# Performance work log

Hardware: AMD Instinct MI355X
Metric: run time of the kernel (lower is better)

Reference implementation:

```python
import jax, jax.numpy as jnp
import numpy as np
from jax.scipy.special import digamma

K = 3
N_CLASSES = 10
HIGH_CST = 1e7


def setup_inputs() -> dict:
    key = jax.random.key(0)
    k1, k2 = jax.random.split(key)
    X = jax.random.normal(k1, (8192, 128), dtype=jnp.float32)
    y = jax.random.randint(k2, (8192,), 0, N_CLASSES, dtype=jnp.int64)
    return {"X": X, "y": y}


def _pairwise_euclidean(X):
    sq = jnp.sum(X * X, axis=1)
    d2 = sq[:, None] - 2.0 * (X @ X.T) + sq[None, :]
    return jnp.sqrt(jnp.maximum(d2, 0.0))


def reference(X, y):
    N = X.shape[0]
    N_digamma = digamma(jnp.asarray(N, dtype=jnp.float32))

    # per-class counts N_x and weighted digamma average
    y32 = y.astype(jnp.int32)
    N_x = jnp.bincount(y32, length=N_CLASSES).astype(jnp.float32)
    avg_N_x = jnp.sum((N_x / N) * digamma(N_x))

    dists = _pairwise_euclidean(X)  # [N, N]

    # mask out different-class pairs with a huge constant
    same_class = y[:, None] == y[None, :]
    dists_same = jnp.where(same_class, dists, HIGH_CST)

    # k-th same-class neighbor distance (self included at distance 0 -> take k+1 smallest, last)
    neg_top, _ = jax.lax.top_k(-dists_same, K + 1)
    anchor_dists = -neg_top[:, -1]  # [N]

    # count all points (any class) within that radius, excluding self
    m_i = jnp.sum(dists <= anchor_dists[:, None], axis=1) - 1
    avg_m_i = jnp.mean(digamma(m_i.astype(jnp.float32)))

    k_digamma = digamma(jnp.asarray(K, dtype=jnp.float32))
    mi = N_digamma - avg_N_x + k_digamma - avg_m_i
    return jnp.maximum(mi / jnp.log(jnp.asarray(2.0, dtype=jnp.float32)), 0.0)
```

## Files before the change

kernel.cpp:

```cpp
#include <hip/hip_runtime.h>
#include <hip/hip_bf16.h>
#include <math.h>

#define NCLS 10
#define NTOT 8192
#define NTIL 64
#define NJT 8
#define NJG (NTOT / (128 * NJT))
#define NPMAX 9472
#define MAXSLOT 32
#define G1 2560

using short8 = __attribute__((ext_vector_type(8))) short;
using f32x4  = __attribute__((ext_vector_type(4))) float;

__device__ __forceinline__ float digammaf_dev(float x) {
    float r = 0.0f;
    while (x < 6.0f) { r -= 1.0f / x; x += 1.0f; }
    float inv = 1.0f / x;
    float inv2 = inv * inv;
    float s = logf(x) - 0.5f * inv
            - inv2 * (0.083333333333f - inv2 * (0.0083333333333f - inv2 * 0.0039682539683f));
    return r + s;
}

__device__ __forceinline__ void cmpswap(float& a, float& b) {
    float lo = fminf(a, b), hi = fmaxf(a, b);
    a = lo; b = hi;
}

__device__ __forceinline__ void ins7(float v, float& b0, float& b1, float& b2, float& b3) {
    float x0 = fminf(b0, v); float c0 = fmaxf(b0, v);
    float x1 = fminf(b1, c0); float c1 = fmaxf(b1, c0);
    float x2 = fminf(b2, c1); float c2 = fmaxf(b2, c1);
    float x3 = fminf(b3, c2);
    b0 = x0; b1 = x1; b2 = x2; b3 = x3;
}

__device__ __forceinline__ void bmerge(int mk, float& v0, float& v1, float& v2, float& v3) {
    float u0 = __shfl_xor(v0, mk), u1 = __shfl_xor(v1, mk);
    float u2 = __shfl_xor(v2, mk), u3 = __shfl_xor(v3, mk);
    float m0 = fminf(v0, u3), m1 = fminf(v1, u2);
    float m2 = fminf(v2, u1), m3 = fminf(v3, u0);
    cmpswap(m0, m2); cmpswap(m1, m3);
    cmpswap(m0, m1); cmpswap(m2, m3);
    v0 = m0; v1 = m1; v2 = m2; v3 = m3;
}

__device__ __forceinline__ void gload_lds16(const void* g, void* s) {
    __builtin_amdgcn_global_load_lds((const __attribute__((address_space(1))) void*)g,
                                     (__attribute__((address_space(3))) void*)s, 16, 0, 0);
}

__global__ void prep_kernel(const float* __restrict__ X,
                            float* __restrict__ sq, unsigned short* __restrict__ XS) {
    int wave = threadIdx.x >> 6, lane = threadIdx.x & 63;
    int row = blockIdx.x * 4 + wave;
    float2 v = *(const float2*)(X + (size_t)row * 128 + lane * 2);
    __hip_bfloat16 h0 = __float2bfloat16(v.x);
    __hip_bfloat16 h1 = __float2bfloat16(v.y);
    float hf0 = __bfloat162float(h0), hf1 = __bfloat162float(h1);
    __hip_bfloat16 l0 = __float2bfloat16(v.x - hf0);
    __hip_bfloat16 l1 = __float2bfloat16(v.y - hf1);
    ushort2 hp, lp;
    hp.x = *(unsigned short*)&h0; hp.y = *(unsigned short*)&h1;
    lp.x = *(unsigned short*)&l0; lp.y = *(unsigned short*)&l1;
    *(ushort2*)(XS + (size_t)row * 256 + lane * 2) = hp;
    *(ushort2*)(XS + (size_t)row * 256 + 128 + lane * 2) = lp;
    float s = fmaf(v.x, v.x, v.y * v.y);
    #pragma unroll
    for (int off = 32; off > 0; off >>= 1) s += __shfl_down(s, off);
    if (lane == 0) sq[row] = s;
}

__global__ void count_kernel(const int* __restrict__ y, int* __restrict__ bcnt) {
    __shared__ int hist[NCLS];
    int t = threadIdx.x;
    if (t < NCLS) hist[t] = 0;
    __syncthreads();
    atomicAdd(&hist[y[blockIdx.x * 256 + t]], 1);
    __syncthreads();
    if (t < NCLS) bcnt[blockIdx.x * NCLS + t] = hist[t];
}

__global__ void plan_kernel(const int* __restrict__ bcnt, int* __restrict__ plan,
                            int* __restrict__ sOff, int* __restrict__ cls) {
    __shared__ int sT[NCLS], sBase[NCLS];
    const int c = threadIdx.x;
    if (c < NCLS) {
        int run = 0;
        #pragma unroll 8
        for (int b = 0; b < 32; ++b) {
            sOff[b * NCLS + c] = run;
            run += bcnt[b * NCLS + c];
        }
        cls[c] = run;
        sT[c] = (run + 127) >> 7;
    }
    __syncthreads();
    if (c == 0) {
        int rowBase = 0, cum = 0;
        for (int q = 0; q < NCLS; ++q) {
            int T = sT[q];
            int nsl = (T + 1) >> 1;
            sBase[q] = rowBase;
            plan[q] = rowBase;
            plan[10 + q] = T;
            plan[20 + q] = nsl;
            plan[30 + q] = cum;
            rowBase += T << 7;
            cum += T * nsl;
        }
        plan[40] = cum;
    }
    __syncthreads();
    if (c < NCLS) {
        int rb = sBase[c];
        #pragma unroll 8
        for (int b = 0; b < 32; ++b) sOff[b * NCLS + c] += rb;
    }
}

__global__ void init_yP(int* __restrict__ yP) {
    yP[blockIdx.x * 256 + threadIdx.x] = -1;
}

__global__ void scatter_kernel(const int* __restrict__ y, const float* __restrict__ sq,
                               const unsigned short* __restrict__ XS,
                               const int* __restrict__ sOff,
                               unsigned short* __restrict__ XSP, float* __restrict__ sqP,
                               int* __restrict__ yP, int* __restrict__ idxP) {
    __shared__ int yloc[256];
    __shared__ int dstloc[256];
    const int b = blockIdx.x, t = threadIdx.x;
    const int gid = b * 256 + t;
    const int yv = y[gid];
    yloc[t] = yv;
    __syncthreads();
    int rank = 0;
    for (int k = 0; k < 256; ++k) rank += (k < t && yloc[k] == yv) ? 1 : 0;
    const int dst = sOff[b * NCLS + yv] + rank;
    dstloc[t] = dst;
    sqP[dst] = sq[gid];
    yP[dst] = yv;
    idxP[dst] = gid;
    __syncthreads();
    const int w = t >> 6, l = t & 63;
    for (int r = w; r < 256; r += 4) {
        int d = dstloc[r];
        *(ushort4*)(XSP + (size_t)d * 256 + l * 4) =
            *(const ushort4*)(XS + (size_t)(b * 256 + r) * 256 + l * 4);
    }
}

__global__ __launch_bounds__(256, 2)
void pass1_kernel(const unsigned short* __restrict__ XSP, const int* __restrict__ yP,
                  const float* __restrict__ sqP, const int* __restrict__ plan,
                  float* __restrict__ top4pP) {
    const int bid = blockIdx.x;
    if (bid >= plan[40]) return;
    __shared__ __align__(16) char smem[65536];

    const int t = threadIdx.x;
    const int w = t >> 6, l = t & 63;
    const int wr = w >> 1, wc = w & 1;
    const int lg = l >> 4, lo16 = l & 15;

    int cc = 0;
    #pragma unroll
    for (int q = 1; q < NCLS; ++q) if (bid >= plan[30 + q]) cc = q;
    const int rowBase = plan[cc], T = plan[10 + cc], nsl = plan[20 + cc];
    const int local = bid - plan[30 + cc];
    const int itile = local / nsl, sIdx = local % nsl;
    const int ibase = rowBase + itile * 128;

    float sqi[16]; int yi[16];
    #pragma unroll
    for (int mi = 0; mi < 4; ++mi)
        #pragma unroll
        for (int r = 0; r < 4; ++r) {
            int row = ibase + wr * 64 + mi * 16 + lg * 4 + r;
            sqi[mi * 4 + r] = sqP[row];
            yi[mi * 4 + r] = yP[row];
        }

    const int swz = (lo16 & 7) << 4;
    unsigned aoff[2], boff[2];
    #pragma unroll
    for (int kk = 0; kk < 2; ++kk) {
        const int cA = (kk * 64 + lg * 16) ^ swz;
        aoff[kk] = (unsigned)((wr * 64 + lo16) * 128 + cA);
        boff[kk] = (unsigned)(32768 + (wc * 64 + lo16) * 128 + cA);
    }
    const int srow = w * 32 + (l >> 3);
    const int scol = ((l & 7) ^ (l >> 3)) << 3;
    const unsigned short* gsrc = XSP + (size_t)srow * 256 + scol;

    auto STAGE = [&](int jbase_rows, int ks, int par) {
        if (ks < 2 || ks >= 4) {
            const int kA = (ks < 4) ? (ks & 1) * 64 : (ks - 2) * 64;
            char* Ab = smem + par * 16384 + w * 4096;
            const unsigned short* gA = gsrc + (size_t)ibase * 256 + kA;
            #pragma unroll
            for (int q = 0; q < 4; ++q)
                gload_lds16(gA + (size_t)q * 8 * 256, Ab + q * 1024);
        }
        const int kB = (ks < 4) ? ks * 64 : (ks - 4) * 64;
        char* Bb = smem + 32768 + par * 16384 + w * 4096;
        const unsigned short* gB = gsrc + (size_t)jbase_rows * 256 + kB;
        #pragma unroll
        for (int q = 0; q < 4; ++q)
            gload_lds16(gB + (size_t)q * 8 * 256, Bb + q * 1024);
    };

    float tp0[16], tp1[16], tp2[16], tp3[16];
    #pragma unroll
    for (int c = 0; c < 16; ++c) {
        tp0[c] = 1e30f; tp1[c] = 1e30f; tp2[c] = 1e30f; tp3[c] = 1e30f;
    }

    STAGE(rowBase + sIdx * 128, 0, 0);
    __syncthreads();

    #pragma unroll 1
    for (int jt = sIdx; jt < T; jt += nsl) {
        const int jbase = rowBase + jt * 128;
        float sqj[4]; int yj[4];
        #pragma unroll
        for (int ni = 0; ni < 4; ++ni) {
            int col = jbase + wc * 64 + ni * 16 + lo16;
            sqj[ni] = sqP[col];
            yj[ni] = yP[col];
        }
        f32x4 acc[4][4];
        f32x4 zz = {0.0f, 0.0f, 0.0f, 0.0f};
        #pragma unroll
        for (int mi = 0; mi < 4; ++mi)
            #pragma unroll
            for (int ni = 0; ni < 4; ++ni) acc[mi][ni] = zz;

        #pragma unroll
        for (int ks = 0; ks < 6; ++ks) {
            const int par = ks & 1;
            if (ks < 5) STAGE(jbase, ks + 1, par ^ 1);
            else if (jt + nsl < T) STAGE(rowBase + (jt + nsl) * 128, 0, par ^ 1);

            #pragma unroll
            for (int kk = 0; kk < 2; ++kk) {
                short8 aF[4], bF[4];
                #pragma unroll
                for (int mi = 0; mi < 4; ++mi)
                    aF[mi] = *(const short8*)(smem + aoff[kk] + par * 16384 + mi * 2048);
                #pragma unroll
                for (int ni = 0; ni < 4; ++ni)
                    bF[ni] = *(const short8*)(smem + boff[kk] + par * 16384 + ni * 2048);
                #pragma unroll
                for (int mi = 0; mi < 4; ++mi)
                    #pragma unroll
                    for (int ni = 0; ni < 4; ++ni)
                        acc[mi][ni] = __builtin_amdgcn_mfma_f32_16x16x32_bf16(
                            aF[mi], bF[ni], acc[mi][ni], 0, 0, 0);
            }

            if (ks == 5) {
                #pragma unroll
                for (int mi = 0; mi < 4; ++mi)
                    #pragma unroll
                    for (int r = 0; r < 4; ++r) {
                        const int idx = mi * 4 + r;
                        #pragma unroll
                        for (int ni = 0; ni < 4; ++ni) {
                            float d2 = fmaf(-2.0f, acc[mi][ni][r], sqi[idx] + sqj[ni]);
                            d2 = fmaxf(d2, 0.0f);
                            float v = (yi[idx] == yj[ni]) ? d2 : 1e30f;
                            ins7(v, tp0[idx], tp1[idx], tp2[idx], tp3[idx]);
                        }
                    }
            }
            __syncthreads();
        }
    }

    float* scrR = (float*)smem;
    #pragma unroll
    for (int idx = 0; idx < 16; ++idx) {
        float v0 = tp0[idx], v1 = tp1[idx], v2 = tp2[idx], v3 = tp3[idx];
        bmerge(1, v0, v1, v2, v3); bmerge(2, v0, v1, v2, v3);
        bmerge(4, v0, v1, v2, v3); bmerge(8, v0, v1, v2, v3);
        if (lo16 == 0) {
            int rl = wr * 64 + (idx >> 2) * 16 + lg * 4 + (idx & 3);
            float4 st; st.x = v0; st.y = v1; st.z = v2; st.w = v3;
            *(float4*)(scrR + rl * 8 + wc * 4) = st;
        }
    }
    __syncthreads();
    if (t < 128) {
        float4 qa = *(float4*)(scrR + t * 8);
        float4 qb = *(float4*)(scrR + t * 8 + 4);
        float b0 = qa.x, b1 = qa.y, b2 = qa.z, b3 = qa.w;
        ins7(qb.x, b0, b1, b2, b3); ins7(qb.y, b0, b1, b2, b3);
        ins7(qb.z, b0, b1, b2, b3); ins7(qb.w, b0, b1, b2, b3);
        size_t base = ((size_t)(ibase + t) * MAXSLOT + sIdx) * 4;
        top4pP[base + 0] = b0; top4pP[base + 1] = b1;
        top4pP[base + 2] = b2; top4pP[base + 3] = b3;
    }
}

__global__ void anchorP_kernel(const float* __restrict__ top4pP, const int* __restrict__ yP,
                               const int* __restrict__ idxP, const int* __restrict__ plan,
                               float* __restrict__ anchor) {
    int r = blockIdx.x * 256 + threadIdx.x;
    int yv = yP[r];
    if (yv < 0) return;
    int nsl = plan[20 + yv];
    float b0 = 1e30f, b1 = 1e30f, b2 = 1e30f, b3 = 1e30f;
    const float4* q4 = (const float4*)(top4pP + (size_t)r * MAXSLOT * 4);
    for (int s = 0; s < nsl; ++s) {
        float4 q = q4[s];
        ins7(q.x, b0, b1, b2, b3); ins7(q.y, b0, b1, b2, b3);
        ins7(q.z, b0, b1, b2, b3); ins7(q.w, b0, b1, b2, b3);
    }
    anchor[idxP[r]] = b3;
}

__global__ __launch_bounds__(256, 2)
void pass2_kernel(const unsigned short* __restrict__ XS, const float* __restrict__ sq,
                  const float* __restrict__ anchor, int* __restrict__ cntp) {
    __shared__ __align__(16) char smem[65536];

    const int t = threadIdx.x;
    const int w = t >> 6, l = t & 63;
    const int wr = w >> 1, wc = w & 1;
    const int lg = l >> 4, lo16 = l & 15;

    const int bid = blockIdx.x;
    const int wg = (bid & 7) * ((NTIL * NJG) >> 3) + (bid >> 3);
    const int it = wg % NTIL, jg = wg / NTIL;
    const int ibase = it * 128;
    const int jg0 = jg * (128 * NJT);

    float sqi[16]; float anc[16];
    #pragma unroll
    for (int mi = 0; mi < 4; ++mi)
        #pragma unroll
        for (int r = 0; r < 4; ++r) {
            int row = ibase + wr * 64 + mi * 16 + lg * 4 + r;
            sqi[mi * 4 + r] = sq[row];
            anc[mi * 4 + r] = anchor[row];
        }

    const int swz = (lo16 & 7) << 4;
    unsigned aoff[2], boff[2];
    #pragma unroll
    for (int kk = 0; kk < 2; ++kk) {
        const int cA = (kk * 64 + lg * 16) ^ swz;
        aoff[kk] = (unsigned)((wr * 64 + lo16) * 128 + cA);
        boff[kk] = (unsigned)(32768 + (wc * 64 + lo16) * 128 + cA);
    }
    const int srow = w * 32 + (l >> 3);
    const int scol = ((l & 7) ^ (l >> 3)) << 3;
    const unsigned short* gsrc = XS + (size_t)srow * 256 + scol;

    auto STAGE = [&](int jbase_rows, int ks, int par) {
        if (ks < 2 || ks >= 4) {
            const int kA = (ks < 4) ? (ks & 1) * 64 : (ks - 2) * 64;
            char* Ab = smem + par * 16384 + w * 4096;
            const unsigned short* gA = gsrc + (size_t)ibase * 256 + kA;
            #pragma unroll
            for (int q = 0; q < 4; ++q)
                gload_lds16(gA + (size_t)q * 8 * 256, Ab + q * 1024);
        }
        const int kB = (ks < 4) ? ks * 64 : (ks - 4) * 64;
        char* Bb = smem + 32768 + par * 16384 + w * 4096;
        const unsigned short* gB = gsrc + (size_t)jbase_rows * 256 + kB;
        #pragma unroll
        for (int q = 0; q < 4; ++q)
            gload_lds16(gB + (size_t)q * 8 * 256, Bb + q * 1024);
    };

    int cnt16[16];
    #pragma unroll
    for (int c = 0; c < 16; ++c) cnt16[c] = 0;

    STAGE(jg0, 0, 0);
    __syncthreads();

    #pragma unroll 1
    for (int jt = 0; jt < NJT; ++jt) {
        const int jbase = jg0 + jt * 128;
        float sqj[4];
        #pragma unroll
        for (int ni = 0; ni < 4; ++ni)
            sqj[ni] = sq[jbase + wc * 64 + ni * 16 + lo16];

        f32x4 acc[4][4];
        f32x4 zz = {0.0f, 0.0f, 0.0f, 0.0f};
        #pragma unroll
        for (int mi = 0; mi < 4; ++mi)
            #pragma unroll
            for (int ni = 0; ni < 4; ++ni) acc[mi][ni] = zz;

        #pragma unroll
        for (int ks = 0; ks < 6; ++ks) {
            const int par = ks & 1;
            if (ks < 5) STAGE(jbase, ks + 1, par ^ 1);
            else if (jt < NJT - 1) STAGE(jbase + 128, 0, par ^ 1);

            #pragma unroll
            for (int kk = 0; kk < 2; ++kk) {
                short8 aF[4], bF[4];
                #pragma unroll
                for (int mi = 0; mi < 4; ++mi)
                    aF[mi] = *(const short8*)(smem + aoff[kk] + par * 16384 + mi * 2048);
                #pragma unroll
                for (int ni = 0; ni < 4; ++ni)
                    bF[ni] = *(const short8*)(smem + boff[kk] + par * 16384 + ni * 2048);
                #pragma unroll
                for (int mi = 0; mi < 4; ++mi)
                    #pragma unroll
                    for (int ni = 0; ni < 4; ++ni)
                        acc[mi][ni] = __builtin_amdgcn_mfma_f32_16x16x32_bf16(
                            aF[mi], bF[ni], acc[mi][ni], 0, 0, 0);
            }

            if (ks == 5) {
                #pragma unroll
                for (int mi = 0; mi < 4; ++mi)
                    #pragma unroll
                    for (int r = 0; r < 4; ++r) {
                        const int idx = mi * 4 + r;
                        int c = 0;
                        #pragma unroll
                        for (int ni = 0; ni < 4; ++ni) {
                            float d2 = fmaf(-2.0f, acc[mi][ni][r], sqi[idx] + sqj[ni]);
                            d2 = fmaxf(d2, 0.0f);
                            c += (d2 <= anc[idx]) ? 1 : 0;
                        }
                        cnt16[idx] += c;
                    }
            }
            __syncthreads();
        }
    }

    int* scri = (int*)smem;
    #pragma unroll
    for (int idx = 0; idx < 16; ++idx) {
        int c = cnt16[idx];
        c += __shfl_xor(c, 1); c += __shfl_xor(c, 2);
        c += __shfl_xor(c, 4); c += __shfl_xor(c, 8);
        if (lo16 == 0) {
            int rl = wr * 64 + (idx >> 2) * 16 + lg * 4 + (idx & 3);
            scri[rl * 2 + wc] = c;
        }
    }
    __syncthreads();
    if (t < 128) cntp[(size_t)(ibase + t) * NJG + jg] = scri[t * 2] + scri[t * 2 + 1];
}

__global__ void reduce_kernel(const int* __restrict__ cntp, float* __restrict__ partials) {
    __shared__ float red[256];
    int t = threadIdx.x;
    int row = blockIdx.x * 256 + t;
    int s = 0;
    for (int c = 0; c < NJG; ++c) s += cntp[(size_t)row * NJG + c];
    red[t] = digammaf_dev((float)(s - 1));
    __syncthreads();
    for (int h = 128; h > 0; h >>= 1) {
        if (t < h) red[t] += red[t + h];
        __syncthreads();
    }
    if (t == 0) partials[blockIdx.x] = red[0];
}

__global__ void finalize_kernel(const float* __restrict__ partials, const int* __restrict__ cls,
                                float* __restrict__ out) {
    if (threadIdx.x == 0) {
        float acc = 0.0f;
        for (int c = 0; c < NTOT / 256; ++c) acc += partials[c];
        float Nf = (float)NTOT;
        float avg_m = acc / Nf;
        float avgNx = 0.0f;
        for (int c = 0; c < NCLS; ++c) {
            float nx = (float)cls[c];
            if (nx > 0.0f) avgNx += (nx / Nf) * digammaf_dev(nx);
        }
        float mi = digammaf_dev(Nf) - avgNx + digammaf_dev(3.0f) - avg_m;
        out[0] = fmaxf(mi / logf(2.0f), 0.0f);
    }
}

extern "C" void kernel_launch(void* const* d_in, const int* in_sizes, int n_in,
                              void* d_out, int out_size, void* d_ws, size_t ws_size,
                              hipStream_t stream) {
    const float* X = (const float*)d_in[0];
    const int* y = (const int*)d_in[1];
    float* out = (float*)d_out;

    float* sq       = (float*)d_ws;
    float* anchors  = sq + NTOT;
    float* partials = anchors + NTOT;
    int*   cls      = (int*)(partials + 32);
    int*   bcnt     = cls + 16;
    int*   sOff     = bcnt + 320;
    int*   plan     = sOff + 320;
    int*   yP       = plan + 48;
    int*   idxP     = yP + NPMAX;
    float* sqP      = (float*)(idxP + NPMAX);
    unsigned short* XS  = (unsigned short*)(sqP + NPMAX);
    unsigned short* XSP = XS + (size_t)NTOT * 256;
    float* top4pP   = (float*)(XSP + (size_t)NPMAX * 256);
    int*   cntp     = (int*)(top4pP + (size_t)NPMAX * MAXSLOT * 4);

    prep_kernel<<<NTOT / 4, 256, 0, stream>>>(X, sq, XS);
    count_kernel<<<NTOT / 256, 256, 0, stream>>>(y, bcnt);
    plan_kernel<<<1, 64, 0, stream>>>(bcnt, plan, sOff, cls);
    init_yP<<<NPMAX / 256, 256, 0, stream>>>(yP);
    scatter_kernel<<<NTOT / 256, 256, 0, stream>>>(y, sq, XS, sOff, XSP, sqP, yP, idxP);
    pass1_kernel<<<G1, 256, 0, stream>>>(XSP, yP, sqP, plan, top4pP);
    anchorP_kernel<<<NPMAX / 256, 256, 0, stream>>>(top4pP, yP, idxP, plan, anchors);
    pass2_kernel<<<NTIL * NJG, 256, 0, stream>>>(XS, sq, anchors, cntp);
    reduce_kernel<<<NTOT / 256, 256, 0, stream>>>(cntp, partials);
    finalize_kernel<<<1, 64, 0, stream>>>(partials, cls, out);
}
```

Baseline: 133.9 us.

## Split pass1 into one block per 64x128 tile pair, fold yP init into plan

Pass1 now launches one block per (64-row i half-tile, 128-col j tile) pair within each class, so it no longer loops over j tiles. The grid grows to 2*T*T blocks per class, the A tile shrinks and LDS drops to 48KB. The goal is more parallelism and occupancy on the GPU and less per-block serial work. The cost is more blocks, repeated B loads and more partial top-4 writes (T slots per row instead of about T/2) that anchorP must merge. The yP initialisation is also folded into plan_kernel, which removes one launch.

```diff
diff --git a/kernel.cpp b/kernel.cpp
--- a/kernel.cpp
+++ b/kernel.cpp
@@ -9,7 +9,7 @@
 #define NJG (NTOT / (128 * NJT))
 #define NPMAX 9472
 #define MAXSLOT 32
-#define G1 2560
+#define G1 3072
 
 using short8 = __attribute__((ext_vector_type(8))) short;
 using f32x4  = __attribute__((ext_vector_type(4))) float;
@@ -84,9 +84,11 @@
 }
 
 __global__ void plan_kernel(const int* __restrict__ bcnt, int* __restrict__ plan,
-                            int* __restrict__ sOff, int* __restrict__ cls) {
+                            int* __restrict__ sOff, int* __restrict__ cls,
+                            int* __restrict__ yP) {
     __shared__ int sT[NCLS], sBase[NCLS];
     const int c = threadIdx.x;
+    for (int i = c; i < NPMAX; i += 256) yP[i] = -1;
     if (c < NCLS) {
         int run = 0;
         #pragma unroll 8
@@ -102,14 +104,13 @@
         int rowBase = 0, cum = 0;
         for (int q = 0; q < NCLS; ++q) {
             int T = sT[q];
-            int nsl = (T + 1) >> 1;
             sBase[q] = rowBase;
             plan[q] = rowBase;
             plan[10 + q] = T;
-            plan[20 + q] = nsl;
+            plan[20 + q] = T;
             plan[30 + q] = cum;
             rowBase += T << 7;
-            cum += T * nsl;
+            cum += 2 * T * T;
         }
         plan[40] = cum;
     }
@@ -119,10 +120,6 @@
         #pragma unroll 8
         for (int b = 0; b < 32; ++b) sOff[b * NCLS + c] += rb;
     }
-}
-
-__global__ void init_yP(int* __restrict__ yP) {
-    yP[blockIdx.x * 256 + threadIdx.x] = -1;
 }
 
 __global__ void scatter_kernel(const int* __restrict__ y, const float* __restrict__ sq,
@@ -159,7 +156,7 @@
                   float* __restrict__ top4pP) {
     const int bid = blockIdx.x;
     if (bid >= plan[40]) return;
-    __shared__ __align__(16) char smem[65536];
+    __shared__ __align__(16) char smem[49152];
 
     const int t = threadIdx.x;
     const int w = t >> 6, l = t & 63;
@@ -169,138 +166,133 @@
     int cc = 0;
     #pragma unroll
     for (int q = 1; q < NCLS; ++q) if (bid >= plan[30 + q]) cc = q;
-    const int rowBase = plan[cc], T = plan[10 + cc], nsl = plan[20 + cc];
+    const int rowBase = plan[cc], T = plan[10 + cc];
     const int local = bid - plan[30 + cc];
-    const int itile = local / nsl, sIdx = local % nsl;
-    const int ibase = rowBase + itile * 128;
-
-    float sqi[16]; int yi[16];
-    #pragma unroll
-    for (int mi = 0; mi < 4; ++mi)
+    const int jt = local % T;
+    const int itile2 = local / T;
+    const int ibase = rowBase + (itile2 >> 1) * 128 + (itile2 & 1) * 64;
+    const int jbase = rowBase + jt * 128;
+
+    float sqi[8]; int yi[8];
+    #pragma unroll
+    for (int mi = 0; mi < 2; ++mi)
         #pragma unroll
         for (int r = 0; r < 4; ++r) {
-            int row = ibase + wr * 64 + mi * 16 + lg * 4 + r;
+            int row = ibase + wr * 32 + mi * 16 + lg * 4 + r;
             sqi[mi * 4 + r] = sqP[row];
             yi[mi * 4 + r] = yP[row];
         }
+    float sqj[4]; int yj[4];
+    #pragma unroll
+    for (int ni = 0; ni < 4; ++ni) {
+        int col = jbase + wc * 64 + ni * 16 + lo16;
+        sqj[ni] = sqP[col];
+        yj[ni] = yP[col];
+    }
 
     const int swz = (lo16 & 7) << 4;
     unsigned aoff[2], boff[2];
     #pragma unroll
     for (int kk = 0; kk < 2; ++kk) {
         const int cA = (kk * 64 + lg * 16) ^ swz;
-        aoff[kk] = (unsigned)((wr * 64 + lo16) * 128 + cA);
-        boff[kk] = (unsigned)(32768 + (wc * 64 + lo16) * 128 + cA);
-    }
-    const int srow = w * 32 + (l >> 3);
+        aoff[kk] = (unsigned)((wr * 32 + lo16) * 128 + cA);
+        boff[kk] = (unsigned)(16384 + (wc * 64 + lo16) * 128 + cA);
+    }
     const int scol = ((l & 7) ^ (l >> 3)) << 3;
-    const unsigned short* gsrc = XSP + (size_t)srow * 256 + scol;
-
-    auto STAGE = [&](int jbase_rows, int ks, int par) {
+    const unsigned short* gsrcA = XSP + (size_t)(w * 16 + (l >> 3)) * 256 + scol;
+    const unsigned short* gsrcB = XSP + (size_t)(w * 32 + (l >> 3)) * 256 + scol;
+
+    auto STAGE = [&](int ks, int par) {
         if (ks < 2 || ks >= 4) {
             const int kA = (ks < 4) ? (ks & 1) * 64 : (ks - 2) * 64;
-            char* Ab = smem + par * 16384 + w * 4096;
-            const unsigned short* gA = gsrc + (size_t)ibase * 256 + kA;
-            #pragma unroll
-            for (int q = 0; q < 4; ++q)
+            char* Ab = smem + par * 8192 + w * 2048;
+            const unsigned short* gA = gsrcA + (size_t)ibase * 256 + kA;
+            #pragma unroll
+            for (int q = 0; q < 2; ++q)
                 gload_lds16(gA + (size_t)q * 8 * 256, Ab + q * 1024);
         }
         const int kB = (ks < 4) ? ks * 64 : (ks - 4) * 64;
-        char* Bb = smem + 32768 + par * 16384 + w * 4096;
-        const unsigned short* gB = gsrc + (size_t)jbase_rows * 256 + kB;
+        char* Bb = smem + 16384 + par * 16384 + w * 4096;
+        const unsigned short* gB = gsrcB + (size_t)jbase * 256 + kB;
         #pragma unroll
         for (int q = 0; q < 4; ++q)
             gload_lds16(gB + (size_t)q * 8 * 256, Bb + q * 1024);
     };
 
-    float tp0[16], tp1[16], tp2[16], tp3[16];
-    #pragma unroll
-    for (int c = 0; c < 16; ++c) {
+    float tp0[8], tp1[8], tp2[8], tp3[8];
+    #pragma unroll
+    for (int c = 0; c < 8; ++c) {
         tp0[c] = 1e30f; tp1[c] = 1e30f; tp2[c] = 1e30f; tp3[c] = 1e30f;
     }
 
-    STAGE(rowBase + sIdx * 128, 0, 0);
-    __syncthreads();
-
-    #pragma unroll 1
-    for (int jt = sIdx; jt < T; jt += nsl) {
-        const int jbase = rowBase + jt * 128;
-        float sqj[4]; int yj[4];
-        #pragma unroll
-        for (int ni = 0; ni < 4; ++ni) {
-            int col = jbase + wc * 64 + ni * 16 + lo16;
-            sqj[ni] = sqP[col];
-            yj[ni] = yP[col];
-        }
-        f32x4 acc[4][4];
-        f32x4 zz = {0.0f, 0.0f, 0.0f, 0.0f};
-        #pragma unroll
-        for (int mi = 0; mi < 4; ++mi)
-            #pragma unroll
-            for (int ni = 0; ni < 4; ++ni) acc[mi][ni] = zz;
-
-        #pragma unroll
-        for (int ks = 0; ks < 6; ++ks) {
-            const int par = ks & 1;
-            if (ks < 5) STAGE(jbase, ks + 1, par ^ 1);
-            else if (jt + nsl < T) STAGE(rowBase + (jt + nsl) * 128, 0, par ^ 1);
-
-            #pragma unroll
-            for (int kk = 0; kk < 2; ++kk) {
-                short8 aF[4], bF[4];
-                #pragma unroll
-                for (int mi = 0; mi < 4; ++mi)
-                    aF[mi] = *(const short8*)(smem + aoff[kk] + par * 16384 + mi * 2048);
+    f32x4 acc[2][4];
+    f32x4 zz = {0.0f, 0.0f, 0.0f, 0.0f};
+    #pragma unroll
+    for (int mi = 0; mi < 2; ++mi)
+        #pragma unroll
+        for (int ni = 0; ni < 4; ++ni) acc[mi][ni] = zz;
+
+    STAGE(0, 0);
+    __syncthreads();
+
+    #pragma unroll
+    for (int ks = 0; ks < 6; ++ks) {
+        const int par = ks & 1;
+        if (ks < 5) STAGE(ks + 1, par ^ 1);
+        #pragma unroll
+        for (int kk = 0; kk < 2; ++kk) {
+            short8 aF[2], bF[4];
+            #pragma unroll
+            for (int mi = 0; mi < 2; ++mi)
+                aF[mi] = *(const short8*)(smem + aoff[kk] + par * 8192 + mi * 2048);
+            #pragma unroll
+            for (int ni = 0; ni < 4; ++ni)
+                bF[ni] = *(const short8*)(smem + boff[kk] + par * 16384 + ni * 2048);
+            #pragma unroll
+            for (int mi = 0; mi < 2; ++mi)
                 #pragma unroll
                 for (int ni = 0; ni < 4; ++ni)
-                    bF[ni] = *(const short8*)(smem + boff[kk] + par * 16384 + ni * 2048);
+                    acc[mi][ni] = __builtin_amdgcn_mfma_f32_16x16x32_bf16(
+                        aF[mi], bF[ni], acc[mi][ni], 0, 0, 0);
+        }
+        if (ks == 5) {
+            #pragma unroll
+            for (int mi = 0; mi < 2; ++mi)
                 #pragma unroll
-                for (int mi = 0; mi < 4; ++mi)
+                for (int r = 0; r < 4; ++r) {
+                    const int idx = mi * 4 + r;
                     #pragma unroll
-                    for (int ni = 0; ni < 4; ++ni)
-                        acc[mi][ni] = __builtin_amdgcn_mfma_f32_16x16x32_bf16(
-                            aF[mi], bF[ni], acc[mi][ni], 0, 0, 0);
-            }
-
-            if (ks == 5) {
-                #pragma unroll
-                for (int mi = 0; mi < 4; ++mi)
-                    #pragma unroll
-                    for (int r = 0; r < 4; ++r) {
-                        const int idx = mi * 4 + r;
-                        #pragma unroll
-                        for (int ni = 0; ni < 4; ++ni) {
-                            float d2 = fmaf(-2.0f, acc[mi][ni][r], sqi[idx] + sqj[ni]);
-                            d2 = fmaxf(d2, 0.0f);
-                            float v = (yi[idx] == yj[ni]) ? d2 : 1e30f;
-                            ins7(v, tp0[idx], tp1[idx], tp2[idx], tp3[idx]);
-                        }
+                    for (int ni = 0; ni < 4; ++ni) {
+                        float d2 = fmaf(-2.0f, acc[mi][ni][r], sqi[idx] + sqj[ni]);
+                        d2 = fmaxf(d2, 0.0f);
+                        float v = (yi[idx] == yj[ni]) ? d2 : 1e30f;
+                        ins7(v, tp0[idx], tp1[idx], tp2[idx], tp3[idx]);
                     }
-            }
-            __syncthreads();
-        }
+                }
+        }
+        __syncthreads();
     }
 
     float* scrR = (float*)smem;
     #pragma unroll
-    for (int idx = 0; idx < 16; ++idx) {
+    for (int idx = 0; idx < 8; ++idx) {
         float v0 = tp0[idx], v1 = tp1[idx], v2 = tp2[idx], v3 = tp3[idx];
         bmerge(1, v0, v1, v2, v3); bmerge(2, v0, v1, v2, v3);
         bmerge(4, v0, v1, v2, v3); bmerge(8, v0, v1, v2, v3);
         if (lo16 == 0) {
-            int rl = wr * 64 + (idx >> 2) * 16 + lg * 4 + (idx & 3);
+            int rl = wr * 32 + (idx >> 2) * 16 + lg * 4 + (idx & 3);
             float4 st; st.x = v0; st.y = v1; st.z = v2; st.w = v3;
             *(float4*)(scrR + rl * 8 + wc * 4) = st;
         }
     }
     __syncthreads();
-    if (t < 128) {
+    if (t < 64) {
         float4 qa = *(float4*)(scrR + t * 8);
         float4 qb = *(float4*)(scrR + t * 8 + 4);
         float b0 = qa.x, b1 = qa.y, b2 = qa.z, b3 = qa.w;
         ins7(qb.x, b0, b1, b2, b3); ins7(qb.y, b0, b1, b2, b3);
         ins7(qb.z, b0, b1, b2, b3); ins7(qb.w, b0, b1, b2, b3);
-        size_t base = ((size_t)(ibase + t) * MAXSLOT + sIdx) * 4;
+        size_t base = ((size_t)(ibase + t) * MAXSLOT + jt) * 4;
         top4pP[base + 0] = b0; top4pP[base + 1] = b1;
         top4pP[base + 2] = b2; top4pP[base + 3] = b3;
     }
@@ -514,8 +506,7 @@
 
     prep_kernel<<<NTOT / 4, 256, 0, stream>>>(X, sq, XS);
     count_kernel<<<NTOT / 256, 256, 0, stream>>>(y, bcnt);
-    plan_kernel<<<1, 64, 0, stream>>>(bcnt, plan, sOff, cls);
-    init_yP<<<NPMAX / 256, 256, 0, stream>>>(yP);
+    plan_kernel<<<1, 256, 0, stream>>>(bcnt, plan, sOff, cls, yP);
     scatter_kernel<<<NTOT / 256, 256, 0, stream>>>(y, sq, XS, sOff, XSP, sqP, yP, idxP);
     pass1_kernel<<<G1, 256, 0, stream>>>(XSP, yP, sqP, plan, top4pP);
     anchorP_kernel<<<NPMAX / 256, 256, 0, stream>>>(top4pP, yP, idxP, plan, anchors);
```

Result: faster. 127.2 us (-5.0%).
